# Kernel tuning notes

Measured on AMD Instinct MI355X. Metric: run time of the kernel, lower is better.

## Reference

```python
import jax, jax.numpy as jnp
import numpy as np

N_HEADS = 8; DH = 64; G = 4; K = 9
C = N_HEADS * DH; CG = C // G
FACTOR = 2.0; TAU = 1.0
SCALE = DH ** -0.5


def _conv1x1(x, w, b):
    # x: (C, *spatial), w: (O, C), b: (O,)
    y = jnp.tensordot(w, x, axes=([1], [0]))
    return y + b.reshape((-1,) + (1,) * (y.ndim - 1))


def _dwconv(x, w, b):
    # depthwise 3x3, SAME padding; x (N,Cg,H,W), w (Cg,1,3,3)
    y = jax.lax.conv_general_dilated(x, w, (1, 1), 'SAME',
                                     feature_group_count=x.shape[1],
                                     dimension_numbers=('NCHW', 'OIHW', 'NCHW'))
    return y + b[None, :, None, None]


def _ln(x, g, b):
    # LayerNormProxy: LN over channel dim of NCHW (torch default eps=1e-5)
    m = jnp.mean(x, axis=1, keepdims=True)
    v = jnp.var(x, axis=1, keepdims=True)
    return (x - m) / jnp.sqrt(v + 1e-5) * g[None, :, None, None] + b[None, :, None, None]


def _grid_sample(img, grid):
    # bilinear, align_corners=True, padding_mode='zeros'
    # img (N,C,H,W), grid (N,Hg,Wg,2) with (x,y) in [-1,1]
    N, Cc, H, W = img.shape
    gx = (grid[..., 0] + 1.0) * 0.5 * (W - 1)
    gy = (grid[..., 1] + 1.0) * 0.5 * (H - 1)
    x0 = jnp.floor(gx); y0 = jnp.floor(gy)

    def g(yy, xx):
        yi = jnp.clip(yy, 0, H - 1).astype(jnp.int32)
        xi = jnp.clip(xx, 0, W - 1).astype(jnp.int32)
        ok = ((yy >= 0) & (yy <= H - 1) & (xx >= 0) & (xx <= W - 1)).astype(img.dtype)
        vals = jax.vmap(lambda im, a, b: im[:, a, b])(img, yi, xi)  # (N,C,Hg,Wg)
        return vals * ok[:, None]

    wx1 = gx - x0; wx0 = 1.0 - wx1
    wy1 = gy - y0; wy0 = 1.0 - wy1
    return (g(y0, x0) * (wy0 * wx0)[:, None]
            + g(y0, x0 + 1) * (wy0 * wx1)[:, None]
            + g(y0 + 1, x0) * (wy1 * wx0)[:, None]
            + g(y0 + 1, x0 + 1) * (wy1 * wx1)[:, None])


def _forward(x, idx, labels, wq, bq, wk, bk, wv, bv, wo, bo,
             ow1, ob1, g1, b1, ow2, ob2, g2, b2, ow3):
    _, _, H, W = x.shape
    n = idx.shape[0]
    iy, ix = idx[:, 0], idx[:, 1]

    q = _conv1x1(x[0], wq, bq)[None]               # (1,C,H,W)
    q_off = q.reshape(G, CG, H, W)                 # (b g) c h w with b=1
    q_sel = q[0][:, iy, ix]                        # (C,n)

    # offset predictor: dwconv -> LN -> GELU (x2) -> 1x1 (no bias)
    t = jax.nn.gelu(_ln(_dwconv(q_off, ow1, ob1), g1, b1), approximate=False)
    t = jax.nn.gelu(_ln(_dwconv(t, ow2, ob2), g2, b2), approximate=False)
    offset = jnp.einsum('gchw,oc->gohw', t, ow3)   # (G,2K,H,W)

    # offset_range_factor > 0: tanh * [1/H,1/W] (tiled K times) * factor
    rng = jnp.tile(jnp.array([1.0 / H, 1.0 / W], offset.dtype), K)
    offset = jnp.tanh(offset) * rng[None, :, None, None] * FACTOR
    off = offset.transpose(0, 2, 3, 1).reshape(G, H, W, K, 2)  # (g,h,w,K,(y,x))

    # reference points in [-1,1] (y,x), unfolded over 3x3 window w/ replication pad
    ry = (jnp.arange(H, dtype=x.dtype) + 0.5) / H * 2.0 - 1.0
    rx = (jnp.arange(W, dtype=x.dtype) + 0.5) / W * 2.0 - 1.0
    ref = jnp.stack(jnp.meshgrid(ry, rx, indexing='ij'), 0)    # (2,H,W)
    pad = jnp.pad(ref, ((0, 0), (1, 1), (1, 1)), mode='edge')
    patches = jnp.stack([pad[:, dy:dy + H, dx:dx + W]
                         for dy in range(3) for dx in range(3)], 0)  # (K,2,H,W)
    ref_unf = patches.transpose(2, 3, 0, 1)                    # (H,W,K,2)

    pos = off + ref_unf[None]                                  # (G,H,W,K,2)
    pos = pos.transpose(0, 3, 1, 2, 4).reshape(G * K, H, W, 2)
    grid = pos[..., ::-1]                                      # (x,y) order

    # gather per-group channels at K learned locations per position
    xg = x.reshape(G, CG, H, W)
    img = jnp.broadcast_to(xg[:, None], (G, K, CG, H, W)).reshape(G * K, CG, H, W)
    xs = _grid_sample(img, grid)                               # (GK,CG,H,W)
    xs = xs.reshape(G, K, CG, H, W).transpose(0, 2, 1, 3, 4).reshape(C, K, H, W)
    xs_sel = xs[:, :, iy, ix]                                  # (C,K,n)

    k = _conv1x1(xs_sel, wk, bk).reshape(N_HEADS, DH, K, n).transpose(0, 1, 3, 2)  # (h,d,n,K)
    v = _conv1x1(xs_sel, wv, bv).reshape(N_HEADS, DH, K, n).transpose(0, 1, 3, 2)
    qh = q_sel.reshape(N_HEADS, DH, n)

    attn = jnp.einsum('hdn,hdnk->hnk', qh, k) * SCALE
    attn = jax.nn.softmax(attn / TAU, axis=-1)                 # (h,n,K)
    out = jnp.einsum('hnk,hdnk->hdn', attn, v).reshape(C, n)
    y = _conv1x1(out, wo, bo).T                                # (n, dim_out)

    sig = jax.nn.sigmoid(y[jnp.arange(n), labels])

    # second grid_sample over full channels at the same learned positions
    img_full = jnp.broadcast_to(x, (G * K, C, H, W))
    xr = _grid_sample(img_full, grid)                          # (GK,C,H,W)
    xr_sel = xr[:, :, iy, ix].transpose(2, 0, 1)               # (n,GK,C)
    return y, attn, xr_sel, sig


def setup_inputs() -> dict:
    key = jax.random.key(0)
    ks = jax.random.split(key, 16)
    H = W = 64; n = 2048; s = 0.02
    return dict(
        x=jax.random.normal(ks[0], (1, C, H, W), jnp.float32),
        idx=jax.random.randint(ks[1], (n, 2), 0, H),
        labels=jax.random.randint(ks[2], (n,), 0, C),
        wq=jax.random.normal(ks[3], (C, C), jnp.float32) * s, bq=jnp.zeros((C,), jnp.float32),
        wk=jax.random.normal(ks[4], (C, C), jnp.float32) * s, bk=jnp.zeros((C,), jnp.float32),
        wv=jax.random.normal(ks[5], (C, C), jnp.float32) * s, bv=jnp.zeros((C,), jnp.float32),
        wo=jax.random.normal(ks[6], (C, C), jnp.float32) * s, bo=jnp.zeros((C,), jnp.float32),
        ow1=jax.random.normal(ks[7], (CG, 1, 3, 3), jnp.float32) * s, ob1=jnp.zeros((CG,), jnp.float32),
        g1=jnp.ones((CG,), jnp.float32), b1=jnp.zeros((CG,), jnp.float32),
        ow2=jax.random.normal(ks[8], (CG, 1, 3, 3), jnp.float32) * s, ob2=jnp.zeros((CG,), jnp.float32),
        g2=jnp.ones((CG,), jnp.float32), b2=jnp.zeros((CG,), jnp.float32),
        ow3=jax.random.normal(ks[9], (2 * K, CG), jnp.float32) * s,
    )


def reference(x, idx, labels, wq, bq, wk, bk, wv, bv, wo, bo,
              ow1, ob1, g1, b1, ow2, ob2, g2, b2, ow3):
    return _forward(x, idx, labels, wq, bq, wk, bk, wv, bv, wo, bo,
                    ow1, ob1, g1, b1, ow2, ob2, g2, b2, ow3)
```

## Files before the change

kernel.cpp:

```cpp
#include <hip/hip_runtime.h>
#include <math.h>

namespace {

typedef unsigned short u16;
typedef unsigned int u32;
typedef __attribute__((ext_vector_type(8))) short bf16x8;
typedef __attribute__((ext_vector_type(4))) float f32x4;
typedef __attribute__((ext_vector_type(2))) float f32x2;

constexpr int HDIM = 64;
constexpr int WDIM = 64;
constexpr int HW = HDIM * WDIM;
constexpr int C = 512;
constexpr int G = 4;
constexpr int CG = 128;
constexpr int K = 9;
constexpr int NH = 8;
constexpr float SCALE = 0.125f;

__device__ __forceinline__ u16 f2b(float f) {
  union { float f; u32 u; } v; v.f = f;
  u32 u = v.u;
  return (u16)((u + 0x7FFFu + ((u >> 16) & 1u)) >> 16);
}
__device__ __forceinline__ float b2f(u16 b) {
  union { u32 u; float f; } v; v.u = ((u32)b) << 16;
  return v.f;
}

__global__ void __launch_bounds__(256)
k_prep(const float* __restrict__ wq, const float* __restrict__ wv,
       const float* __restrict__ wo, const float* __restrict__ wk,
       const float* __restrict__ x,
       u16* __restrict__ wqb, u16* __restrict__ wvb, u16* __restrict__ wob,
       u16* __restrict__ wkT, u16* __restrict__ xtb) {
  int b = blockIdx.x;
  int t = threadIdx.x;
  if (b < 1024) {
    int j = b * 256 + t;
    wqb[j] = f2b(wq[j]);
    wvb[j] = f2b(wv[j]);
    wob[j] = f2b(wo[j]);
    return;
  }
  __shared__ float tile[32][33];
  int tx = t & 31, ty = t >> 5;
  if (b < 1280) {
    int bb = b - 1024;
    int r0 = (bb & 15) * 32, c0 = (bb >> 4) * 32;
    for (int r = ty; r < 32; r += 8) tile[r][tx] = wk[(r0 + r) * C + c0 + tx];
    __syncthreads();
    for (int r = ty; r < 32; r += 8) wkT[(c0 + r) * C + r0 + tx] = f2b(tile[tx][r]);
  } else {
    int bb = b - 1280;
    int p0 = (bb & 127) * 32, c0 = (bb >> 7) * 32;
    for (int r = ty; r < 32; r += 8) tile[r][tx] = x[(c0 + r) * HW + p0 + tx];
    __syncthreads();
    for (int r = ty; r < 32; r += 8) xtb[(p0 + r) * C + c0 + tx] = f2b(tile[tx][r]);
  }
}

template <bool OUT_BF16>
__global__ void __launch_bounds__(256)
k_gemm_mfma(const u16* __restrict__ A, int lda, int aOffZ,
            const int* __restrict__ aIdx,
            const u16* __restrict__ BT, int ldb, int bOffZ,
            const float* __restrict__ bias, int biasOffZ,
            void* __restrict__ Dp, int ldd, int dOffZ, int Kd,
            const int* __restrict__ labels, float* __restrict__ sigp) {
  int z = blockIdx.z;
  const u16* Ab = A + (size_t)z * aOffZ;
  const u16* Bb = BT + (size_t)z * bOffZ;
  int t = threadIdx.x;
  int wave = t >> 6, lane = t & 63;
  int wm = (wave >> 1) * 32, wn = (wave & 1) * 32;
  int bm = blockIdx.x * 64 + wm;
  int bn = blockIdx.y * 64 + wn;
  int row = lane & 15, quad = lane >> 4;
  size_t ar[2];
#pragma unroll
  for (int mt = 0; mt < 2; ++mt) {
    int r = bm + mt * 16 + row;
    ar[mt] = aIdx ? (size_t)(aIdx[2 * r] * WDIM + aIdx[2 * r + 1]) : (size_t)r;
  }
  f32x4 acc[2][2] = {};
  for (int k0 = 0; k0 < Kd; k0 += 32) {
    bf16x8 a[2], b[2];
#pragma unroll
    for (int mt = 0; mt < 2; ++mt)
      a[mt] = *(const bf16x8*)&Ab[ar[mt] * lda + k0 + quad * 8];
#pragma unroll
    for (int nt = 0; nt < 2; ++nt)
      b[nt] = *(const bf16x8*)&Bb[(size_t)(bn + nt * 16 + row) * ldb + k0 + quad * 8];
#pragma unroll
    for (int mt = 0; mt < 2; ++mt)
#pragma unroll
      for (int nt = 0; nt < 2; ++nt)
        acc[mt][nt] = __builtin_amdgcn_mfma_f32_16x16x32_bf16(a[mt], b[nt], acc[mt][nt], 0, 0, 0);
  }
#pragma unroll
  for (int nt = 0; nt < 2; ++nt) {
    int cc = bn + nt * 16 + row;
    float bb = bias ? bias[(size_t)z * biasOffZ + cc] : 0.0f;
#pragma unroll
    for (int mt = 0; mt < 2; ++mt)
#pragma unroll
      for (int r = 0; r < 4; ++r) {
        int rr = bm + mt * 16 + quad * 4 + r;
        float v = acc[mt][nt][r] + bb;
        if (OUT_BF16) {
          ((u16*)Dp)[(size_t)z * dOffZ + (size_t)rr * ldd + cc] = f2b(v);
        } else {
          ((float*)Dp)[(size_t)z * dOffZ + (size_t)rr * ldd + cc] = v;
          if (labels && labels[rr] == cc) sigp[rr] = 1.0f / (1.0f + expf(-v));
        }
      }
  }
}

__global__ void __launch_bounds__(256)
k_dwln2(const u16* __restrict__ in, const float* __restrict__ w9,
        const float* __restrict__ wb, const float* __restrict__ lng,
        const float* __restrict__ lnb, u16* __restrict__ outp) {
  int p = blockIdx.x;
  int h = p >> 6, w = p & 63;
  int t = threadIdx.x;
  int c0 = t * 2;
  int cg0 = c0 & 127, cg1 = cg0 + 1;
  float a0 = wb[cg0], a1 = wb[cg1];
#pragma unroll
  for (int dy = 0; dy < 3; ++dy) {
    int hh = h + dy - 1;
    if (hh < 0 || hh >= HDIM) continue;
#pragma unroll
    for (int dx = 0; dx < 3; ++dx) {
      int ww = w + dx - 1;
      if (ww < 0 || ww >= WDIM) continue;
      u32 pr2 = *(const u32*)&in[(hh * WDIM + ww) * C + c0];
      float wt0 = w9[cg0 * 9 + dy * 3 + dx];
      float wt1 = w9[cg1 * 9 + dy * 3 + dx];
      a0 += wt0 * b2f((u16)pr2);
      a1 += wt1 * b2f((u16)(pr2 >> 16));
    }
  }
  float s = a0 + a1, s2 = a0 * a0 + a1 * a1;
#pragma unroll
  for (int o = 32; o > 0; o >>= 1) {
    s += __shfl_xor(s, o, 64);
    s2 += __shfl_xor(s2, o, 64);
  }
  float mean = s * (1.0f / 128.0f);
  float var = s2 * (1.0f / 128.0f) - mean * mean;
  float rstd = rsqrtf(var + 1e-5f);
  float xn0 = (a0 - mean) * rstd * lng[cg0] + lnb[cg0];
  float xn1 = (a1 - mean) * rstd * lng[cg1] + lnb[cg1];
  u16 o0 = f2b(0.5f * xn0 * (1.0f + erff(xn0 * 0.70710678f)));
  u16 o1 = f2b(0.5f * xn1 * (1.0f + erff(xn1 * 0.70710678f)));
  *(u32*)&outp[(size_t)p * C + c0] = ((u32)o1 << 16) | o0;
}

__global__ void __launch_bounds__(128)
k_offsets2(const u16* __restrict__ t2, const float* __restrict__ ow3,
           const int* __restrict__ idx, float* __restrict__ pos) {
  int i = blockIdx.x;
  int t = threadIdx.x;
  int iy = idx[2 * i], ix = idx[2 * i + 1];
  int p = iy * WDIM + ix;
  __shared__ float tl[512];
  __shared__ float ov[72];
#pragma unroll
  for (int j = 0; j < 4; ++j) tl[t + 128 * j] = b2f(t2[(size_t)p * C + t + 128 * j]);
  __syncthreads();
  if (t < 72) {
    int g = t / 18, l = t % 18;
    float a = 0.0f;
#pragma unroll 4
    for (int j = 0; j < 128; ++j) a += ow3[l * CG + j] * tl[g * CG + j];
    ov[t] = a;
  }
  __syncthreads();
  if (t < 36) {
    int g = t / 9, l = t % 9;
    int dy = l / 3, dx = l % 3;
    int ryi = min(max(iy + dy - 1, 0), HDIM - 1);
    int rxi = min(max(ix + dx - 1, 0), WDIM - 1);
    float ry = (ryi + 0.5f) * (2.0f / HDIM) - 1.0f;
    float rx = (rxi + 0.5f) * (2.0f / WDIM) - 1.0f;
    float py = tanhf(ov[g * 18 + 2 * l]) * (2.0f / HDIM) + ry;
    float px = tanhf(ov[g * 18 + 2 * l + 1]) * (2.0f / WDIM) + rx;
    int o = ((i * G + g) * K + l) * 2;
    pos[o] = py;
    pos[o + 1] = px;
  }
}

__global__ void __launch_bounds__(256)
k_attn3(const u16* __restrict__ qk2b, const u16* __restrict__ xtb,
        const float* __restrict__ pos, float* __restrict__ attn_out,
        u16* __restrict__ z2b, float* __restrict__ xr, int n) {
  constexpr int LD = 520;
  int i = blockIdx.x;
  int t = threadIdx.x;
  __shared__ alignas(16) u16 qkl[16 * LD];
  __shared__ alignas(16) u16 xsl[16 * LD];
  __shared__ int ro[36][4];
  __shared__ float wbl[36][4];
  __shared__ float lg[NH][K];
  __shared__ float pr[NH][K];
  {
    const bf16x8* qs = (const bf16x8*)(qk2b + (size_t)i * (NH * C));
#pragma unroll
    for (int cix = t; cix < 512; cix += 256) {
      bf16x8 val = qs[cix];
      int r = cix >> 6;
      int co = (cix & 63) * 8;
      *(bf16x8*)&qkl[r * LD + co] = val;
    }
  }
  if (t < 36) {
    float py = pos[(size_t)i * 72 + 2 * t];
    float px = pos[(size_t)i * 72 + 2 * t + 1];
    float gx = (px + 1.0f) * 0.5f * (WDIM - 1);
    float gy = (py + 1.0f) * 0.5f * (HDIM - 1);
    float x0f = floorf(gx), y0f = floorf(gy);
    float wx1 = gx - x0f, wx0 = 1.0f - wx1;
    float wy1 = gy - y0f, wy0 = 1.0f - wy1;
    int x0 = (int)x0f, y0 = (int)y0f;
    int x1 = x0 + 1, y1 = y0 + 1;
    bool vx0 = (x0 >= 0) && (x0 < WDIM);
    bool vx1 = (x1 >= 0) && (x1 < WDIM);
    bool vy0 = (y0 >= 0) && (y0 < HDIM);
    bool vy1 = (y1 >= 0) && (y1 < HDIM);
    wbl[t][0] = (vy0 && vx0) ? wy0 * wx0 : 0.0f;
    wbl[t][1] = (vy0 && vx1) ? wy0 * wx1 : 0.0f;
    wbl[t][2] = (vy1 && vx0) ? wy1 * wx0 : 0.0f;
    wbl[t][3] = (vy1 && vx1) ? wy1 * wx1 : 0.0f;
    int x0c = min(max(x0, 0), WDIM - 1), x1c = min(max(x1, 0), WDIM - 1);
    int y0c = min(max(y0, 0), HDIM - 1), y1c = min(max(y1, 0), HDIM - 1);
    ro[t][0] = (y0c * WDIM + x0c) * C;
    ro[t][1] = (y0c * WDIM + x1c) * C;
    ro[t][2] = (y1c * WDIM + x0c) * C;
    ro[t][3] = (y1c * WDIM + x1c) * C;
  }
  __syncthreads();
  int wave = t >> 6;
  int c2 = t * 2;
  float* xrb = xr + (size_t)i * (G * K) * C;
#pragma unroll 1
  for (int g = 0; g < G; ++g) {
#pragma unroll 3
    for (int kk = 0; kk < K; ++kk) {
      int it = g * K + kk;
      float w00 = wbl[it][0], w01 = wbl[it][1], w10 = wbl[it][2], w11 = wbl[it][3];
      u32 a00 = *(const u32*)&xtb[ro[it][0] + c2];
      u32 a01 = *(const u32*)&xtb[ro[it][1] + c2];
      u32 a10 = *(const u32*)&xtb[ro[it][2] + c2];
      u32 a11 = *(const u32*)&xtb[ro[it][3] + c2];
      float v0 = w00 * b2f((u16)a00) + w01 * b2f((u16)a01) +
                 w10 * b2f((u16)a10) + w11 * b2f((u16)a11);
      float v1 = w00 * b2f((u16)(a00 >> 16)) + w01 * b2f((u16)(a01 >> 16)) +
                 w10 * b2f((u16)(a10 >> 16)) + w11 * b2f((u16)(a11 >> 16));
      f32x2 ov = {v0, v1};
      __builtin_nontemporal_store(ov, (f32x2*)&xrb[(size_t)it * C + c2]);
      if (wave == g) *(u32*)&xsl[kk * LD + c2] = ((u32)f2b(v1) << 16) | f2b(v0);
    }
  }
  __syncthreads();
  if (wave == 0) {
    int lane = t & 63;
    int row = lane & 15, quad = lane >> 4;
    f32x4 acc = {};
#pragma unroll 4
    for (int k0 = 0; k0 < C; k0 += 32) {
      bf16x8 a = *(const bf16x8*)&qkl[row * LD + k0 + quad * 8];
      bf16x8 b = *(const bf16x8*)&xsl[row * LD + k0 + quad * 8];
      acc = __builtin_amdgcn_mfma_f32_16x16x32_bf16(a, b, acc, 0, 0, 0);
    }
    if (row < K && quad < 2) {
#pragma unroll
      for (int r = 0; r < 4; ++r) lg[quad * 4 + r][row] = acc[r] * SCALE;
    }
  }
  __syncthreads();
  if (t < NH) {
    float mx = -1e30f;
    for (int kk = 0; kk < K; ++kk) mx = fmaxf(mx, lg[t][kk]);
    float sm = 0.0f;
    float e[K];
    for (int kk = 0; kk < K; ++kk) { e[kk] = expf(lg[t][kk] - mx); sm += e[kk]; }
    float inv = 1.0f / sm;
    for (int kk = 0; kk < K; ++kk) {
      float p = e[kk] * inv;
      pr[t][kk] = p;
      attn_out[((size_t)t * n + i) * K + kk] = p;
    }
  }
  __syncthreads();
  {
    int h = t >> 5;
    int cbase = (t & 31) * 16;
    float prr[K];
#pragma unroll
    for (int kk = 0; kk < K; ++kk) prr[kk] = pr[h][kk];
    float accz[16] = {};
#pragma unroll
    for (int kk = 0; kk < K; ++kk) {
      bf16x8 v0 = *(const bf16x8*)&xsl[kk * LD + cbase];
      bf16x8 v1 = *(const bf16x8*)&xsl[kk * LD + cbase + 8];
      float p = prr[kk];
#pragma unroll
      for (int e = 0; e < 8; ++e) {
        accz[e] += p * b2f((u16)v0[e]);
        accz[8 + e] += p * b2f((u16)v1[e]);
      }
    }
    u16 ob[16];
#pragma unroll
    for (int e = 0; e < 16; ++e) ob[e] = f2b(accz[e]);
    u16* zdst = z2b + (size_t)i * (NH * C) + h * C + cbase;
    *(bf16x8*)&zdst[0] = *(const bf16x8*)&ob[0];
    *(bf16x8*)&zdst[8] = *(const bf16x8*)&ob[8];
  }
}

}

extern "C" void kernel_launch(void* const* d_in, const int* in_sizes, int n_in,
                              void* d_out, int out_size, void* d_ws, size_t ws_size,
                              hipStream_t stream) {
  (void)n_in; (void)out_size; (void)ws_size;
  const float* x = (const float*)d_in[0];
  const int* idx = (const int*)d_in[1];
  const int* labels = (const int*)d_in[2];
  const float* wq = (const float*)d_in[3];
  const float* bq = (const float*)d_in[4];
  const float* wk = (const float*)d_in[5];
  const float* wv = (const float*)d_in[7];
  const float* bv = (const float*)d_in[8];
  const float* wo = (const float*)d_in[9];
  const float* bo = (const float*)d_in[10];
  const float* ow1 = (const float*)d_in[11];
  const float* ob1 = (const float*)d_in[12];
  const float* g1 = (const float*)d_in[13];
  const float* b1 = (const float*)d_in[14];
  const float* ow2 = (const float*)d_in[15];
  const float* ob2 = (const float*)d_in[16];
  const float* g2 = (const float*)d_in[17];
  const float* b2 = (const float*)d_in[18];
  const float* ow3 = (const float*)d_in[19];
  int n = in_sizes[1] / 2;

  unsigned char* wp = (unsigned char*)d_ws;
  auto alloc = [&](size_t bytes) {
    unsigned char* p = wp;
    wp += (bytes + 255) & ~(size_t)255;
    return p;
  };
  u16* xtb = (u16*)alloc((size_t)HW * C * 2);
  u16* wqb = (u16*)alloc((size_t)C * C * 2);
  u16* wvb = (u16*)alloc((size_t)C * C * 2);
  u16* wob = (u16*)alloc((size_t)C * C * 2);
  u16* wkT = (u16*)alloc((size_t)C * C * 2);
  u16* q_tb = (u16*)alloc((size_t)HW * C * 2);
  u16* t1b = (u16*)alloc((size_t)HW * C * 2);
  u16* t2b = (u16*)alloc((size_t)HW * C * 2);
  u16* qk2b = (u16*)alloc((size_t)n * NH * C * 2);
  float* pos = (float*)alloc((size_t)n * G * K * 2 * 4);
  u16* z2b = (u16*)alloc((size_t)n * NH * C * 2);
  u16* outb = (u16*)alloc((size_t)n * C * 2);

  float* out_f = (float*)d_out;
  float* y_out = out_f;
  float* attn_out = y_out + (size_t)n * C;
  float* xr_out = attn_out + (size_t)NH * n * K;
  float* sig_out = xr_out + (size_t)n * G * K * C;

  k_prep<<<dim3(3328), 256, 0, stream>>>(wq, wv, wo, wk, x, wqb, wvb, wob, wkT, xtb);

  k_gemm_mfma<true><<<dim3(HW / 64, C / 64, 1), 256, 0, stream>>>(
      xtb, C, 0, nullptr, wqb, C, 0, bq, 0, q_tb, C, 0, C, nullptr, nullptr);

  k_dwln2<<<dim3(HW), 256, 0, stream>>>(q_tb, ow1, ob1, g1, b1, t1b);
  k_dwln2<<<dim3(HW), 256, 0, stream>>>(t1b, ow2, ob2, g2, b2, t2b);
  k_offsets2<<<dim3(n), 128, 0, stream>>>(t2b, ow3, idx, pos);

  k_gemm_mfma<true><<<dim3(n / 64, C / 64, NH), 256, 0, stream>>>(
      q_tb, C, 64, idx, wkT, C, 64, nullptr, 0, qk2b, NH * C, C, 64, nullptr, nullptr);

  k_attn3<<<dim3(n), 256, 0, stream>>>(qk2b, xtb, pos, attn_out, z2b, xr_out, n);

  k_gemm_mfma<true><<<dim3(n / 64, 1, NH), 256, 0, stream>>>(
      z2b, NH * C, C, nullptr, wvb, C, 64 * C, bv, 64, outb, C, 64, C, nullptr, nullptr);

  k_gemm_mfma<false><<<dim3(n / 64, C / 64, 1), 256, 0, stream>>>(
      outb, C, 0, nullptr, wob, C, 0, bo, 0, y_out, C, 0, C, labels, sig_out);
}
```

Baseline: 326.3 us.

## Fuse second dwconv+LN+GELU into offset kernel, computing only at query points

The second depthwise conv/LayerNorm/GELU pass used to run over all 4096 pixels and write a full bf16 map. It is now computed only at the n selected query positions, inside a fused kernel that also does the 1x1 offset projection with wave shuffles. This removes a full-image kernel, its intermediate buffer and the separate offsets launch. Separately, the bilinear sampling loop in the attention kernel now loads 4 channels per thread and splits sampling points across two block halves, giving wider loads and stores.

```diff
diff --git a/kernel.cpp b/kernel.cpp
--- a/kernel.cpp
+++ b/kernel.cpp
@@ -8,6 +8,7 @@
 typedef __attribute__((ext_vector_type(8))) short bf16x8;
 typedef __attribute__((ext_vector_type(4))) float f32x4;
 typedef __attribute__((ext_vector_type(2))) float f32x2;
+typedef __attribute__((ext_vector_type(2))) unsigned int u32x2;
 
 constexpr int HDIM = 64;
 constexpr int WDIM = 64;
@@ -160,38 +161,68 @@
   *(u32*)&outp[(size_t)p * C + c0] = ((u32)o1 << 16) | o0;
 }
 
-__global__ void __launch_bounds__(128)
-k_offsets2(const u16* __restrict__ t2, const float* __restrict__ ow3,
-           const int* __restrict__ idx, float* __restrict__ pos) {
+__global__ void __launch_bounds__(256)
+k_dwoff(const u16* __restrict__ t1, const float* __restrict__ w9,
+        const float* __restrict__ wb, const float* __restrict__ lng,
+        const float* __restrict__ lnb, const float* __restrict__ ow3,
+        const int* __restrict__ idx, float* __restrict__ pos) {
   int i = blockIdx.x;
   int t = threadIdx.x;
   int iy = idx[2 * i], ix = idx[2 * i + 1];
-  int p = iy * WDIM + ix;
-  __shared__ float tl[512];
-  __shared__ float ov[72];
-#pragma unroll
-  for (int j = 0; j < 4; ++j) tl[t + 128 * j] = b2f(t2[(size_t)p * C + t + 128 * j]);
-  __syncthreads();
-  if (t < 72) {
-    int g = t / 18, l = t % 18;
-    float a = 0.0f;
-#pragma unroll 4
-    for (int j = 0; j < 128; ++j) a += ow3[l * CG + j] * tl[g * CG + j];
-    ov[t] = a;
-  }
-  __syncthreads();
-  if (t < 36) {
-    int g = t / 9, l = t % 9;
-    int dy = l / 3, dx = l % 3;
+  int c0 = t * 2;
+  int cg0 = c0 & 127, cg1 = cg0 + 1;
+  int g = t >> 6;
+  int lane = t & 63;
+  float a0 = wb[cg0], a1 = wb[cg1];
+#pragma unroll
+  for (int dy = 0; dy < 3; ++dy) {
+    int hh = iy + dy - 1;
+    if (hh < 0 || hh >= HDIM) continue;
+#pragma unroll
+    for (int dx = 0; dx < 3; ++dx) {
+      int ww = ix + dx - 1;
+      if (ww < 0 || ww >= WDIM) continue;
+      u32 pr2 = *(const u32*)&t1[(hh * WDIM + ww) * C + c0];
+      float wt0 = w9[cg0 * 9 + dy * 3 + dx];
+      float wt1 = w9[cg1 * 9 + dy * 3 + dx];
+      a0 += wt0 * b2f((u16)pr2);
+      a1 += wt1 * b2f((u16)(pr2 >> 16));
+    }
+  }
+  float s = a0 + a1, s2 = a0 * a0 + a1 * a1;
+#pragma unroll
+  for (int o = 32; o > 0; o >>= 1) {
+    s += __shfl_xor(s, o, 64);
+    s2 += __shfl_xor(s2, o, 64);
+  }
+  float mean = s * (1.0f / 128.0f);
+  float var = s2 * (1.0f / 128.0f) - mean * mean;
+  float rstd = rsqrtf(var + 1e-5f);
+  float xn0 = (a0 - mean) * rstd * lng[cg0] + lnb[cg0];
+  float xn1 = (a1 - mean) * rstd * lng[cg1] + lnb[cg1];
+  float x0 = 0.5f * xn0 * (1.0f + erff(xn0 * 0.70710678f));
+  float x1 = 0.5f * xn1 * (1.0f + erff(xn1 * 0.70710678f));
+  float ovreg = 0.0f;
+#pragma unroll
+  for (int l = 0; l < 18; ++l) {
+    float a = ow3[l * CG + cg0] * x0 + ow3[l * CG + cg1] * x1;
+#pragma unroll
+    for (int o = 32; o > 0; o >>= 1) a += __shfl_xor(a, o, 64);
+    if (lane == l) ovreg = a;
+  }
+  int ls = (lane < 9) ? lane : 0;
+  float vy = __shfl(ovreg, 2 * ls, 64);
+  float vx = __shfl(ovreg, 2 * ls + 1, 64);
+  if (lane < 9) {
+    int dy = lane / 3, dx = lane % 3;
     int ryi = min(max(iy + dy - 1, 0), HDIM - 1);
     int rxi = min(max(ix + dx - 1, 0), WDIM - 1);
     float ry = (ryi + 0.5f) * (2.0f / HDIM) - 1.0f;
     float rx = (rxi + 0.5f) * (2.0f / WDIM) - 1.0f;
-    float py = tanhf(ov[g * 18 + 2 * l]) * (2.0f / HDIM) + ry;
-    float px = tanhf(ov[g * 18 + 2 * l + 1]) * (2.0f / WDIM) + rx;
-    int o = ((i * G + g) * K + l) * 2;
-    pos[o] = py;
-    pos[o + 1] = px;
+    f32x2 pv;
+    pv.x = tanhf(vy) * (2.0f / HDIM) + ry;
+    pv.y = tanhf(vx) * (2.0f / WDIM) + rx;
+    *(f32x2*)&pos[((i * G + g) * K + lane) * 2] = pv;
   }
 }
 
@@ -245,25 +276,37 @@
   }
   __syncthreads();
   int wave = t >> 6;
-  int c2 = t * 2;
   float* xrb = xr + (size_t)i * (G * K) * C;
-#pragma unroll 1
-  for (int g = 0; g < G; ++g) {
+  {
+    int half = t >> 7;
+    int th = t & 127;
+    int c4 = th * 4;
 #pragma unroll 3
-    for (int kk = 0; kk < K; ++kk) {
-      int it = g * K + kk;
+    for (int j = 0; j < 18; ++j) {
+      int it = 2 * j + half;
       float w00 = wbl[it][0], w01 = wbl[it][1], w10 = wbl[it][2], w11 = wbl[it][3];
-      u32 a00 = *(const u32*)&xtb[ro[it][0] + c2];
-      u32 a01 = *(const u32*)&xtb[ro[it][1] + c2];
-      u32 a10 = *(const u32*)&xtb[ro[it][2] + c2];
-      u32 a11 = *(const u32*)&xtb[ro[it][3] + c2];
-      float v0 = w00 * b2f((u16)a00) + w01 * b2f((u16)a01) +
-                 w10 * b2f((u16)a10) + w11 * b2f((u16)a11);
-      float v1 = w00 * b2f((u16)(a00 >> 16)) + w01 * b2f((u16)(a01 >> 16)) +
-                 w10 * b2f((u16)(a10 >> 16)) + w11 * b2f((u16)(a11 >> 16));
-      f32x2 ov = {v0, v1};
-      __builtin_nontemporal_store(ov, (f32x2*)&xrb[(size_t)it * C + c2]);
-      if (wave == g) *(u32*)&xsl[kk * LD + c2] = ((u32)f2b(v1) << 16) | f2b(v0);
+      u32x2 q00 = *(const u32x2*)&xtb[ro[it][0] + c4];
+      u32x2 q01 = *(const u32x2*)&xtb[ro[it][1] + c4];
+      u32x2 q10 = *(const u32x2*)&xtb[ro[it][2] + c4];
+      u32x2 q11 = *(const u32x2*)&xtb[ro[it][3] + c4];
+      float v0 = w00 * b2f((u16)q00.x) + w01 * b2f((u16)q01.x) +
+                 w10 * b2f((u16)q10.x) + w11 * b2f((u16)q11.x);
+      float v1 = w00 * b2f((u16)(q00.x >> 16)) + w01 * b2f((u16)(q01.x >> 16)) +
+                 w10 * b2f((u16)(q10.x >> 16)) + w11 * b2f((u16)(q11.x >> 16));
+      float v2 = w00 * b2f((u16)q00.y) + w01 * b2f((u16)q01.y) +
+                 w10 * b2f((u16)q10.y) + w11 * b2f((u16)q11.y);
+      float v3 = w00 * b2f((u16)(q00.y >> 16)) + w01 * b2f((u16)(q01.y >> 16)) +
+                 w10 * b2f((u16)(q10.y >> 16)) + w11 * b2f((u16)(q11.y >> 16));
+      f32x4 ov = {v0, v1, v2, v3};
+      __builtin_nontemporal_store(ov, (f32x4*)&xrb[(size_t)it * C + c4]);
+      int gi = (it * 57) >> 9;
+      if ((th >> 5) == gi) {
+        int kk = it - gi * 9;
+        u32x2 pk;
+        pk.x = ((u32)f2b(v1) << 16) | f2b(v0);
+        pk.y = ((u32)f2b(v3) << 16) | f2b(v2);
+        *(u32x2*)&xsl[kk * LD + c4] = pk;
+      }
     }
   }
   __syncthreads();
@@ -364,7 +407,6 @@
   u16* wkT = (u16*)alloc((size_t)C * C * 2);
   u16* q_tb = (u16*)alloc((size_t)HW * C * 2);
   u16* t1b = (u16*)alloc((size_t)HW * C * 2);
-  u16* t2b = (u16*)alloc((size_t)HW * C * 2);
   u16* qk2b = (u16*)alloc((size_t)n * NH * C * 2);
   float* pos = (float*)alloc((size_t)n * G * K * 2 * 4);
   u16* z2b = (u16*)alloc((size_t)n * NH * C * 2);
@@ -382,8 +424,7 @@
       xtb, C, 0, nullptr, wqb, C, 0, bq, 0, q_tb, C, 0, C, nullptr, nullptr);
 
   k_dwln2<<<dim3(HW), 256, 0, stream>>>(q_tb, ow1, ob1, g1, b1, t1b);
-  k_dwln2<<<dim3(HW), 256, 0, stream>>>(t1b, ow2, ob2, g2, b2, t2b);
-  k_offsets2<<<dim3(n), 128, 0, stream>>>(t2b, ow3, idx, pos);
+  k_dwoff<<<dim3(n), 256, 0, stream>>>(t1b, ow2, ob2, g2, b2, ow3, idx, pos);
 
   k_gemm_mfma<true><<<dim3(n / 64, C / 64, NH), 256, 0, stream>>>(
       q_tb, C, 64, idx, wkT, C, 64, nullptr, 0, qk2b, NH * C, C, 64, nullptr, nullptr);
```

Measured after the change: 305.5 us. 1.07x faster.
